# Kernel optimization log

Measured on AMD Instinct MI355X. Metric: run time of the kernel, lower is better.

The kernel has to match this reference:

```python
import jax, jax.numpy as jnp
import numpy as np
from jax import lax

B, NP = 4, 8192          # events, points per event (equal-sized batches)
RATIO, R, K = 0.25, 0.2, 64
MP = int(NP * RATIO)     # sampled centers per event
D_IN = 32
BIG = 1e10


def _fps_one(pos):
    # Farthest point sampling (deterministic start at index 0). pos: [NP,3] -> [MP] int32
    d = jnp.sum((pos - pos[0]) ** 2, axis=-1)
    sel = jnp.zeros((MP,), jnp.int32)

    def body(i, carry):
        sel, d = carry
        nxt = jnp.argmax(d).astype(jnp.int32)
        sel = sel.at[i].set(nxt)
        d = jnp.minimum(d, jnp.sum((pos - pos[nxt]) ** 2, axis=-1))
        return sel, d

    sel, _ = lax.fori_loop(1, MP, body, (sel, d))
    return sel


def _ball_query_one(centers, pos):
    # centers: [MP,3], pos: [NP,3] -> neighbor idx [MP,K] int32, validity mask [MP,K]
    d2 = jnp.sum((centers[:, None, :] - pos[None, :, :]) ** 2, axis=-1)  # [MP,NP]
    d2m = jnp.where(d2 <= R * R, d2, BIG)
    neg, idx = lax.top_k(-d2m, K)          # K nearest within radius (deterministic)
    mask = (-neg) <= R * R
    return idx.astype(jnp.int32), mask


def reference(x, pos, batch, W1, b1, W2, b2, W3, b3):
    xb = x.reshape(B, NP, D_IN)
    pb = pos.reshape(B, NP, 3)

    sel = jax.vmap(_fps_one)(pb)                                   # [B,MP]
    centers = jnp.take_along_axis(pb, sel[..., None], axis=1)      # [B,MP,3]
    idx, mask = jax.vmap(_ball_query_one)(centers, pb)             # [B,MP,K]

    gather = jax.vmap(lambda a, i: a[i])
    pos_j = gather(pb, idx)                                        # [B,MP,K,3]
    x_j = gather(xb, idx)                                          # [B,MP,K,D_IN]

    rel = pos_j - centers[:, :, None, :]
    h = jnp.concatenate([x_j, rel], axis=-1)                       # [B,MP,K,D_IN+3]
    h = jax.nn.relu(h @ W1 + b1)
    h = jax.nn.relu(h @ W2 + b2)
    h = jax.nn.relu(h @ W3 + b3)                                   # [B,MP,K,128]

    h = jnp.where(mask[..., None], h, -BIG)
    x_out = jnp.max(h, axis=2).reshape(B * MP, -1)                 # max aggregation
    pos_out = centers.reshape(B * MP, 3)
    batch_out = jnp.repeat(jnp.arange(B, dtype=jnp.int32), MP)
    return x_out, pos_out, batch_out


def setup_inputs() -> dict:
    key = jax.random.key(0)
    ks = jax.random.split(key, 8)
    x = jax.random.normal(ks[0], (B * NP, D_IN), jnp.float32)
    pos = jax.random.uniform(ks[1], (B * NP, 3), jnp.float32)
    batch = (jnp.arange(B * NP) // NP).astype(jnp.int64)
    W1 = jax.random.normal(ks[2], (D_IN + 3, 64), jnp.float32) * 0.05
    b1 = jnp.zeros((64,), jnp.float32)
    W2 = jax.random.normal(ks[3], (64, 64), jnp.float32) * 0.05
    b2 = jnp.zeros((64,), jnp.float32)
    W3 = jax.random.normal(ks[4], (64, 128), jnp.float32) * 0.05
    b3 = jnp.zeros((128,), jnp.float32)
    return {"x": x, "pos": pos, "batch": batch, "W1": W1, "b1": b1,
            "W2": W2, "b2": b2, "W3": W3, "b3": b3}
```

## Files before the change

### kernel.cpp

```cpp
#include <hip/hip_runtime.h>


#define BATCH 4
#define NP 8192
#define MP 2048
#define KNN 64
#define DIN 32
#define PPL 32

#define DPP_FMAX(v, ctrl)                                                     \
  {                                                                           \
    int _t = __builtin_amdgcn_update_dpp(__float_as_int(v),                   \
                                         __float_as_int(v), (ctrl), 0xF,      \
                                         0xF, false);                         \
    (v) = fmaxf((v), __int_as_float(_t));                                     \
  }

#define DPP_MINU(v, ctrl)                                                     \
  {                                                                           \
    unsigned _t = (unsigned)__builtin_amdgcn_update_dpp((int)(v), (int)(v),   \
                                                        (ctrl), 0xF, 0xF,    \
                                                        false);               \
    (v) = ((v) < _t) ? (v) : _t;                                              \
  }

typedef float v2f __attribute__((ext_vector_type(2)));

__global__ __launch_bounds__(256, 1) void fps_k(const float* __restrict__ pos,
                                                const float* __restrict__ x,
                                                const float* __restrict__ W1,
                                                const float* __restrict__ W2,
                                                const float* __restrict__ W3,
                                                float* __restrict__ pout,
                                                float* __restrict__ bout,
                                                float* __restrict__ P1,
                                                float* __restrict__ W2T,
                                                float* __restrict__ W3T)
{
  const int bid = blockIdx.x;
  const int tid = threadIdx.x;

  if (bid >= BATCH) {
    if (bid < BATCH + 8192) {
      const int j = (bid - BATCH) * 4 + (tid >> 6);
      const int c = tid & 63;
      const float* __restrict__ xr = x + (size_t)j * DIN;
      float acc = 0.f;
#pragma unroll
      for (int k = 0; k < DIN; k++) acc += xr[k] * W1[k * 64 + c];
      P1[(size_t)j * 64 + c] = acc;
    } else {
      const int e = (bid - (BATCH + 8192)) * 256 + tid;
      if (e < 64 * 64) {
        const int c = e >> 6, k = e & 63;
        W2T[e] = W2[k * 64 + c];
      } else {
        const int e2 = e - 64 * 64;
        const int c = e2 >> 6, k = e2 & 63;
        W3T[e2] = W3[k * 128 + c];
      }
    }
    return;
  }

  const int b = bid;
  const int lane = tid & 63, wid = tid >> 6;
  const float* __restrict__ pb = pos + (size_t)b * NP * 3;
  const int base = tid * PPL;

#pragma unroll
  for (int q = 0; q < 8; q++) bout[b * MP + q * 256 + tid] = (float)b;

  __shared__ __align__(16) float ptab[NP * 3];
  __shared__ unsigned long long slt[2][4];

  {
    float4* __restrict__ pt4 = (float4*)ptab;
    const float4* __restrict__ pv4 = (const float4*)pb;
#pragma unroll
    for (int q = 0; q < 24; q++) pt4[q * 256 + tid] = pv4[q * 256 + tid];
  }

  const float c0x = pb[0], c0y = pb[1], c0z = pb[2];
  if (tid == 0) {
    pout[(size_t)b * MP * 3 + 0] = c0x;
    pout[(size_t)b * MP * 3 + 1] = c0y;
    pout[(size_t)b * MP * 3 + 2] = c0z;
  }
  __syncthreads();

  v2f px[16], py[16], pz[16], d[16];
#pragma unroll
  for (int j = 0; j < 16; j++) {
    const float* __restrict__ pp = &ptab[tid * (PPL * 3) + j * 6];
    const v2f A = *(const v2f*)&pp[0];
    const v2f Bv = *(const v2f*)&pp[2];
    const v2f C = *(const v2f*)&pp[4];
    px[j].x = A.x;  px[j].y = Bv.y;
    py[j].x = A.y;  py[j].y = C.x;
    pz[j].x = Bv.x; pz[j].y = C.y;
  }

  float bv = -1.f;
  {
    const v2f cx = {c0x, c0x}, cy = {c0y, c0y}, cz = {c0z, c0z};
#pragma unroll
    for (int j = 0; j < 16; j++) {
      v2f dx = px[j] - cx, dy = py[j] - cy, dz = pz[j] - cz;
      v2f nd = dx * dx + dy * dy + dz * dz;
      d[j] = nd;
      bv = fmaxf(fmaxf(nd.x, nd.y), bv);
    }
  }

  for (int i = 1; i < MP; i++) {
    float v = bv;
    DPP_FMAX(v, 0x111);
    DPP_FMAX(v, 0x112);
    DPP_FMAX(v, 0x114);
    DPP_FMAX(v, 0x118);
    DPP_FMAX(v, 0x142);
    DPP_FMAX(v, 0x143);
    const float wmax =
        __int_as_float(__builtin_amdgcn_readlane(__float_as_int(v), 63));

    const unsigned long long m = __ballot(bv == wmax);
    const int src = (int)__builtin_ctzll(m);
    const int p = i & 1;
    if (lane == src) {
      int ks = PPL - 1;
#pragma unroll
      for (int k = PPL - 2; k >= 0; k--) {
        const float dv = (k & 1) ? d[k >> 1].y : d[k >> 1].x;
        if (dv == wmax) ks = k;
      }
      slt[p][wid] = ((unsigned long long)__float_as_uint(wmax) << 32)
                    | (unsigned)(base + ks);
    }
    __syncthreads();

    const unsigned long long kv = slt[p][lane & 3];
    const float v2 = __uint_as_float((unsigned)(kv >> 32));
    float v2r = v2;
    DPP_FMAX(v2r, 0x111);
    DPP_FMAX(v2r, 0x112);
    const float mv =
        __int_as_float(__builtin_amdgcn_readlane(__float_as_int(v2r), 3));
    const unsigned long long m2 = __ballot(v2 == mv);
    const int mw = (int)__builtin_ctzll(m2);
    const int js = __builtin_amdgcn_readlane((int)(unsigned)kv, mw);
    const float ncx = ptab[js * 3 + 0];
    const float ncy = ptab[js * 3 + 1];
    const float ncz = ptab[js * 3 + 2];

    if (tid == 0) {
      pout[((size_t)b * MP + i) * 3 + 0] = ncx;
      pout[((size_t)b * MP + i) * 3 + 1] = ncy;
      pout[((size_t)b * MP + i) * 3 + 2] = ncz;
    }

    const v2f cx = {ncx, ncx}, cy = {ncy, ncy}, cz = {ncz, ncz};
    bv = -1.f;
#pragma unroll
    for (int j = 0; j < 16; j++) {
      v2f dx = px[j] - cx, dy = py[j] - cy, dz = pz[j] - cz;
      v2f nd = dx * dx + dy * dy + dz * dz;
      v2f dn;
      dn.x = fminf(d[j].x, nd.x);
      dn.y = fminf(d[j].y, nd.y);
      d[j] = dn;
      bv = fmaxf(fmaxf(dn.x, dn.y), bv);
    }
  }
}

__global__ __launch_bounds__(64) void ballq_k(const float* __restrict__ pos,
                                              const float* __restrict__ pout,
                                              int* __restrict__ nbr)
{
  const int wg = blockIdx.x;
  const int lane = threadIdx.x;
  const int b = wg >> 11;
  const float* __restrict__ pb = pos + (size_t)b * NP * 3;
  const float cx = pout[(size_t)wg * 3 + 0];
  const float cy = pout[(size_t)wg * 3 + 1];
  const float cz = pout[(size_t)wg * 3 + 2];
  const float R2 = (float)(0.2 * 0.2);

  __shared__ unsigned long long cand[1024];
  int cnt = 0;
  for (int basej = 0; basej < NP; basej += 64) {
    const int j = basej + lane;
    float dx = pb[j * 3 + 0] - cx;
    float dy = pb[j * 3 + 1] - cy;
    float dz = pb[j * 3 + 2] - cz;
    float d2 = dx * dx + dy * dy + dz * dz;
    bool in = (d2 <= R2);
    unsigned long long mb = __ballot(in);
    int pre = (int)__popcll(mb & ((1ull << lane) - 1ull));
    int slot = cnt + pre;
    if (in && slot < 1024)
      cand[slot] = ((unsigned long long)__float_as_uint(d2) << 32) | (unsigned int)j;
    cnt += (int)__popcll(mb);
  }
  if (cnt > 1024) cnt = 1024;

  unsigned long long last = 0;
  int myout = -1;
  for (int r = 0; r < KNN; r++) {
    unsigned long long v = ~0ull;
    for (int s = lane; s < cnt; s += 64) {
      const unsigned long long c = cand[s];
      if (c >= last && c < v) v = c;
    }
    const unsigned hi = (unsigned)(v >> 32);
    unsigned h = hi;
    DPP_MINU(h, 0x111);
    DPP_MINU(h, 0x112);
    DPP_MINU(h, 0x114);
    DPP_MINU(h, 0x118);
    DPP_MINU(h, 0x142);
    DPP_MINU(h, 0x143);
    const unsigned mhi = (unsigned)__builtin_amdgcn_readlane((int)h, 63);
    const unsigned lo = (hi == mhi) ? (unsigned)v : 0xffffffffu;
    unsigned l2 = lo;
    DPP_MINU(l2, 0x111);
    DPP_MINU(l2, 0x112);
    DPP_MINU(l2, 0x114);
    DPP_MINU(l2, 0x118);
    DPP_MINU(l2, 0x142);
    DPP_MINU(l2, 0x143);
    const unsigned mlo = (unsigned)__builtin_amdgcn_readlane((int)l2, 63);

    if (lane == r) myout = (mhi == 0xffffffffu) ? -1 : (int)mlo;
    last = (mhi == 0xffffffffu)
               ? ~0ull
               : ((((unsigned long long)mhi << 32) | mlo) + 1ull);
  }
  nbr[(size_t)wg * KNN + lane] = myout;
}

__global__ __launch_bounds__(64) void mlp_k(const float* __restrict__ pos,
    const float* __restrict__ P1, const float* __restrict__ W1,
    const float* __restrict__ b1, const float* __restrict__ W2T,
    const float* __restrict__ b2, const float* __restrict__ W3T,
    const float* __restrict__ b3, const int* __restrict__ nbr,
    const float* __restrict__ pout, float* __restrict__ xout)
{
  __shared__ __align__(16) float h2s[64 * 68];
  const int wg = blockIdx.x;
  const int lane = threadIdx.x;
  const int b = wg >> 11;
  const int idx = nbr[(size_t)wg * KNN + lane];
  const bool valid = idx >= 0;
  const int j = valid ? idx : 0;
  const float cx = pout[(size_t)wg * 3 + 0];
  const float cy = pout[(size_t)wg * 3 + 1];
  const float cz = pout[(size_t)wg * 3 + 2];
  const float* __restrict__ pj = pos + ((size_t)b * NP + j) * 3;
  const float rx = pj[0] - cx, ry = pj[1] - cy, rz = pj[2] - cz;
  const float* __restrict__ p1r =
      (const float*)__builtin_assume_aligned(P1 + ((size_t)b * NP + j) * 64, 16);

  float h1[64];
#pragma unroll
  for (int k = 0; k < 64; k++) {
    float v = p1r[k] + rx * W1[32 * 64 + k] + ry * W1[33 * 64 + k]
                     + rz * W1[34 * 64 + k] + b1[k];
    h1[k] = fmaxf(v, 0.f);
  }

  for (int c4 = 0; c4 < 16; c4++) {
    float a0 = b2[c4 * 4 + 0], a1 = b2[c4 * 4 + 1];
    float a2 = b2[c4 * 4 + 2], a3 = b2[c4 * 4 + 3];
    const float* __restrict__ w0 = W2T + (c4 * 4 + 0) * 64;
    const float* __restrict__ w1 = W2T + (c4 * 4 + 1) * 64;
    const float* __restrict__ w2 = W2T + (c4 * 4 + 2) * 64;
    const float* __restrict__ w3 = W2T + (c4 * 4 + 3) * 64;
#pragma unroll
    for (int k = 0; k < 64; k++) {
      a0 += h1[k] * w0[k]; a1 += h1[k] * w1[k];
      a2 += h1[k] * w2[k]; a3 += h1[k] * w3[k];
    }
    float4 q;
    q.x = fmaxf(a0, 0.f); q.y = fmaxf(a1, 0.f);
    q.z = fmaxf(a2, 0.f); q.w = fmaxf(a3, 0.f);
    *(float4*)&h2s[lane * 68 + c4 * 4] = q;
  }

  float4 keep = make_float4(0.f, 0.f, 0.f, 0.f);
  const float* __restrict__ h2p = &h2s[lane * 68];
  for (int c4 = 0; c4 < 32; c4++) {
    float a0 = b3[c4 * 4 + 0], a1 = b3[c4 * 4 + 1];
    float a2 = b3[c4 * 4 + 2], a3 = b3[c4 * 4 + 3];
    const float* __restrict__ w0 = W3T + (c4 * 4 + 0) * 64;
    const float* __restrict__ w1 = W3T + (c4 * 4 + 1) * 64;
    const float* __restrict__ w2 = W3T + (c4 * 4 + 2) * 64;
    const float* __restrict__ w3 = W3T + (c4 * 4 + 3) * 64;
#pragma unroll
    for (int k4 = 0; k4 < 16; k4++) {
      float4 h = *(const float4*)&h2p[k4 * 4];
      a0 += h.x * w0[k4 * 4 + 0]; a0 += h.y * w0[k4 * 4 + 1];
      a0 += h.z * w0[k4 * 4 + 2]; a0 += h.w * w0[k4 * 4 + 3];
      a1 += h.x * w1[k4 * 4 + 0]; a1 += h.y * w1[k4 * 4 + 1];
      a1 += h.z * w1[k4 * 4 + 2]; a1 += h.w * w1[k4 * 4 + 3];
      a2 += h.x * w2[k4 * 4 + 0]; a2 += h.y * w2[k4 * 4 + 1];
      a2 += h.z * w2[k4 * 4 + 2]; a2 += h.w * w2[k4 * 4 + 3];
      a3 += h.x * w3[k4 * 4 + 0]; a3 += h.y * w3[k4 * 4 + 1];
      a3 += h.z * w3[k4 * 4 + 2]; a3 += h.w * w3[k4 * 4 + 3];
    }
    a0 = valid ? fmaxf(a0, 0.f) : 0.f;
    a1 = valid ? fmaxf(a1, 0.f) : 0.f;
    a2 = valid ? fmaxf(a2, 0.f) : 0.f;
    a3 = valid ? fmaxf(a3, 0.f) : 0.f;
#pragma unroll
    for (int off = 1; off < 64; off <<= 1) {
      a0 = fmaxf(a0, __shfl_xor(a0, off));
      a1 = fmaxf(a1, __shfl_xor(a1, off));
      a2 = fmaxf(a2, __shfl_xor(a2, off));
      a3 = fmaxf(a3, __shfl_xor(a3, off));
    }
    if (lane == c4) { keep.x = a0; keep.y = a1; keep.z = a2; keep.w = a3; }
  }
  if (lane < 32)
    *(float4*)&xout[(size_t)wg * 128 + lane * 4] = keep;
}

extern "C" void kernel_launch(void* const* d_in, const int* in_sizes, int n_in,
                              void* d_out, int out_size, void* d_ws, size_t ws_size,
                              hipStream_t stream)
{
  const float* x   = (const float*)d_in[0];
  const float* pos = (const float*)d_in[1];
  const float* W1 = (const float*)d_in[3];
  const float* b1 = (const float*)d_in[4];
  const float* W2 = (const float*)d_in[5];
  const float* b2 = (const float*)d_in[6];
  const float* W3 = (const float*)d_in[7];
  const float* b3 = (const float*)d_in[8];

  float* out  = (float*)d_out;
  float* xout = out;
  float* pout = out + 8192 * 128;
  float* bout = out + 8192 * 128 + 8192 * 3;

  char* ws = (char*)d_ws;
  float* P1  = (float*)ws;
  float* W2T = (float*)(ws + 8388608);
  float* W3T = (float*)(ws + 8404992);
  int*   nbr = (int*)(ws + 8437760);

  fps_k<<<dim3(BATCH + 8192 + 48), dim3(256), 0, stream>>>(
      pos, x, W1, W2, W3, pout, bout, P1, W2T, W3T);
  ballq_k<<<dim3(BATCH * MP), dim3(64), 0, stream>>>(pos, pout, nbr);
  mlp_k<<<dim3(BATCH * MP), dim3(64), 0, stream>>>(pos, P1, W1, b1, W2T, b2,
                                                   W3T, b3, nbr, pout, xout);
}
```

Before: 2.693 ms.

## Widen FPS to 1024 threads per event and fuse ball query with MLP

Farthest point sampling now uses 1024 threads per event, 8 points each, instead of 256 threads with 32 points each. This cuts the per-iteration serial distance update and argmax scan, at the cost of a wider 16-wave cross-wave reduction. The ball-query and MLP kernels are merged into one, with shared memory reused between them, so the neighbor index buffer round trip and one launch go away. The P1 precompute and weight-transpose blocks are regridded to match the 1024-thread block size.

```diff
diff --git a/kernel.cpp b/kernel.cpp
--- a/kernel.cpp
+++ b/kernel.cpp
@@ -6,7 +6,6 @@
 #define MP 2048
 #define KNN 64
 #define DIN 32
-#define PPL 32
 
 #define DPP_FMAX(v, ctrl)                                                     \
   {                                                                           \
@@ -26,23 +25,23 @@
 
 typedef float v2f __attribute__((ext_vector_type(2)));
 
-__global__ __launch_bounds__(256, 1) void fps_k(const float* __restrict__ pos,
-                                                const float* __restrict__ x,
-                                                const float* __restrict__ W1,
-                                                const float* __restrict__ W2,
-                                                const float* __restrict__ W3,
-                                                float* __restrict__ pout,
-                                                float* __restrict__ bout,
-                                                float* __restrict__ P1,
-                                                float* __restrict__ W2T,
-                                                float* __restrict__ W3T)
+__global__ __launch_bounds__(1024) void fps_k(const float* __restrict__ pos,
+                                              const float* __restrict__ x,
+                                              const float* __restrict__ W1,
+                                              const float* __restrict__ W2,
+                                              const float* __restrict__ W3,
+                                              float* __restrict__ pout,
+                                              float* __restrict__ bout,
+                                              float* __restrict__ P1,
+                                              float* __restrict__ W2T,
+                                              float* __restrict__ W3T)
 {
   const int bid = blockIdx.x;
   const int tid = threadIdx.x;
 
   if (bid >= BATCH) {
-    if (bid < BATCH + 8192) {
-      const int j = (bid - BATCH) * 4 + (tid >> 6);
+    if (bid < BATCH + 2048) {
+      const int j = (bid - BATCH) * 16 + (tid >> 6);
       const int c = tid & 63;
       const float* __restrict__ xr = x + (size_t)j * DIN;
       float acc = 0.f;
@@ -50,14 +49,17 @@
       for (int k = 0; k < DIN; k++) acc += xr[k] * W1[k * 64 + c];
       P1[(size_t)j * 64 + c] = acc;
     } else {
-      const int e = (bid - (BATCH + 8192)) * 256 + tid;
-      if (e < 64 * 64) {
-        const int c = e >> 6, k = e & 63;
-        W2T[e] = W2[k * 64 + c];
-      } else {
-        const int e2 = e - 64 * 64;
-        const int c = e2 >> 6, k = e2 & 63;
-        W3T[e2] = W3[k * 128 + c];
+#pragma unroll
+      for (int it = 0; it < 12; it++) {
+        const int e = it * 1024 + tid;
+        if (e < 64 * 64) {
+          const int c = e >> 6, k = e & 63;
+          W2T[e] = W2[k * 64 + c];
+        } else {
+          const int e2 = e - 64 * 64;
+          const int c = e2 >> 6, k = e2 & 63;
+          W3T[e2] = W3[k * 128 + c];
+        }
       }
     }
     return;
@@ -66,19 +68,26 @@
   const int b = bid;
   const int lane = tid & 63, wid = tid >> 6;
   const float* __restrict__ pb = pos + (size_t)b * NP * 3;
-  const int base = tid * PPL;
-
-#pragma unroll
-  for (int q = 0; q < 8; q++) bout[b * MP + q * 256 + tid] = (float)b;
+  const int base = tid * 8;
+
+  bout[b * MP + tid] = (float)b;
+  bout[b * MP + 1024 + tid] = (float)b;
 
   __shared__ __align__(16) float ptab[NP * 3];
-  __shared__ unsigned long long slt[2][4];
-
-  {
-    float4* __restrict__ pt4 = (float4*)ptab;
-    const float4* __restrict__ pv4 = (const float4*)pb;
-#pragma unroll
-    for (int q = 0; q < 24; q++) pt4[q * 256 + tid] = pv4[q * 256 + tid];
+  __shared__ unsigned long long slt[2][16];
+
+  float t[24];
+  const float4* __restrict__ pv = (const float4*)(pb + (size_t)tid * 24);
+#pragma unroll
+  for (int q = 0; q < 6; q++) *(float4*)&t[q * 4] = pv[q];
+#pragma unroll
+  for (int q = 0; q < 6; q++) *(float4*)&ptab[tid * 24 + q * 4] = *(float4*)&t[q * 4];
+
+  v2f px[4], py[4], pz[4], d[4];
+#pragma unroll
+  for (int j = 0; j < 4; j++) {
+    px[j].x = t[6 * j + 0]; py[j].x = t[6 * j + 1]; pz[j].x = t[6 * j + 2];
+    px[j].y = t[6 * j + 3]; py[j].y = t[6 * j + 4]; pz[j].y = t[6 * j + 5];
   }
 
   const float c0x = pb[0], c0y = pb[1], c0z = pb[2];
@@ -87,29 +96,16 @@
     pout[(size_t)b * MP * 3 + 1] = c0y;
     pout[(size_t)b * MP * 3 + 2] = c0z;
   }
-  __syncthreads();
-
-  v2f px[16], py[16], pz[16], d[16];
-#pragma unroll
-  for (int j = 0; j < 16; j++) {
-    const float* __restrict__ pp = &ptab[tid * (PPL * 3) + j * 6];
-    const v2f A = *(const v2f*)&pp[0];
-    const v2f Bv = *(const v2f*)&pp[2];
-    const v2f C = *(const v2f*)&pp[4];
-    px[j].x = A.x;  px[j].y = Bv.y;
-    py[j].x = A.y;  py[j].y = C.x;
-    pz[j].x = Bv.x; pz[j].y = C.y;
-  }
 
   float bv = -1.f;
   {
-    const v2f cx = {c0x, c0x}, cy = {c0y, c0y}, cz = {c0z, c0z};
-#pragma unroll
-    for (int j = 0; j < 16; j++) {
+    v2f cx = {c0x, c0x}, cy = {c0y, c0y}, cz = {c0z, c0z};
+#pragma unroll
+    for (int j = 0; j < 4; j++) {
       v2f dx = px[j] - cx, dy = py[j] - cy, dz = pz[j] - cz;
       v2f nd = dx * dx + dy * dy + dz * dz;
       d[j] = nd;
-      bv = fmaxf(fmaxf(nd.x, nd.y), bv);
+      bv = fmaxf(bv, fmaxf(nd.x, nd.y));
     }
   }
 
@@ -128,10 +124,10 @@
     const int src = (int)__builtin_ctzll(m);
     const int p = i & 1;
     if (lane == src) {
-      int ks = PPL - 1;
-#pragma unroll
-      for (int k = PPL - 2; k >= 0; k--) {
-        const float dv = (k & 1) ? d[k >> 1].y : d[k >> 1].x;
+      int ks = 7;
+#pragma unroll
+      for (int k = 6; k >= 0; k--) {
+        float dv = (k & 1) ? d[k >> 1].y : d[k >> 1].x;
         if (dv == wmax) ks = k;
       }
       slt[p][wid] = ((unsigned long long)__float_as_uint(wmax) << 32)
@@ -139,13 +135,15 @@
     }
     __syncthreads();
 
-    const unsigned long long kv = slt[p][lane & 3];
+    const unsigned long long kv = slt[p][lane & 15];
     const float v2 = __uint_as_float((unsigned)(kv >> 32));
     float v2r = v2;
     DPP_FMAX(v2r, 0x111);
     DPP_FMAX(v2r, 0x112);
+    DPP_FMAX(v2r, 0x114);
+    DPP_FMAX(v2r, 0x118);
     const float mv =
-        __int_as_float(__builtin_amdgcn_readlane(__float_as_int(v2r), 3));
+        __int_as_float(__builtin_amdgcn_readlane(__float_as_int(v2r), 15));
     const unsigned long long m2 = __ballot(v2 == mv);
     const int mw = (int)__builtin_ctzll(m2);
     const int js = __builtin_amdgcn_readlane((int)(unsigned)kv, mw);
@@ -162,22 +160,28 @@
     const v2f cx = {ncx, ncx}, cy = {ncy, ncy}, cz = {ncz, ncz};
     bv = -1.f;
 #pragma unroll
-    for (int j = 0; j < 16; j++) {
+    for (int j = 0; j < 4; j++) {
       v2f dx = px[j] - cx, dy = py[j] - cy, dz = pz[j] - cz;
       v2f nd = dx * dx + dy * dy + dz * dz;
       v2f dn;
       dn.x = fminf(d[j].x, nd.x);
       dn.y = fminf(d[j].y, nd.y);
       d[j] = dn;
-      bv = fmaxf(fmaxf(dn.x, dn.y), bv);
+      bv = fmaxf(bv, fmaxf(dn.x, dn.y));
     }
   }
 }
 
-__global__ __launch_bounds__(64) void ballq_k(const float* __restrict__ pos,
-                                              const float* __restrict__ pout,
-                                              int* __restrict__ nbr)
+__global__ __launch_bounds__(64) void bqmlp_k(const float* __restrict__ pos,
+    const float* __restrict__ P1, const float* __restrict__ W1,
+    const float* __restrict__ b1, const float* __restrict__ W2T,
+    const float* __restrict__ b2, const float* __restrict__ W3T,
+    const float* __restrict__ b3, const float* __restrict__ pout,
+    float* __restrict__ xout)
 {
+  __shared__ __align__(16) float smem[64 * 68];
+  unsigned long long* __restrict__ cand = (unsigned long long*)smem;
+
   const int wg = blockIdx.x;
   const int lane = threadIdx.x;
   const int b = wg >> 11;
@@ -187,7 +191,6 @@
   const float cz = pout[(size_t)wg * 3 + 2];
   const float R2 = (float)(0.2 * 0.2);
 
-  __shared__ unsigned long long cand[1024];
   int cnt = 0;
   for (int basej = 0; basej < NP; basej += 64) {
     const int j = basej + lane;
@@ -237,26 +240,12 @@
                ? ~0ull
                : ((((unsigned long long)mhi << 32) | mlo) + 1ull);
   }
-  nbr[(size_t)wg * KNN + lane] = myout;
-}
-
-__global__ __launch_bounds__(64) void mlp_k(const float* __restrict__ pos,
-    const float* __restrict__ P1, const float* __restrict__ W1,
-    const float* __restrict__ b1, const float* __restrict__ W2T,
-    const float* __restrict__ b2, const float* __restrict__ W3T,
-    const float* __restrict__ b3, const int* __restrict__ nbr,
-    const float* __restrict__ pout, float* __restrict__ xout)
-{
-  __shared__ __align__(16) float h2s[64 * 68];
-  const int wg = blockIdx.x;
-  const int lane = threadIdx.x;
-  const int b = wg >> 11;
-  const int idx = nbr[(size_t)wg * KNN + lane];
+
+  __syncthreads();
+
+  const int idx = myout;
   const bool valid = idx >= 0;
   const int j = valid ? idx : 0;
-  const float cx = pout[(size_t)wg * 3 + 0];
-  const float cy = pout[(size_t)wg * 3 + 1];
-  const float cz = pout[(size_t)wg * 3 + 2];
   const float* __restrict__ pj = pos + ((size_t)b * NP + j) * 3;
   const float rx = pj[0] - cx, ry = pj[1] - cy, rz = pj[2] - cz;
   const float* __restrict__ p1r =
@@ -285,11 +274,11 @@
     float4 q;
     q.x = fmaxf(a0, 0.f); q.y = fmaxf(a1, 0.f);
     q.z = fmaxf(a2, 0.f); q.w = fmaxf(a3, 0.f);
-    *(float4*)&h2s[lane * 68 + c4 * 4] = q;
+    *(float4*)&smem[lane * 68 + c4 * 4] = q;
   }
 
   float4 keep = make_float4(0.f, 0.f, 0.f, 0.f);
-  const float* __restrict__ h2p = &h2s[lane * 68];
+  const float* __restrict__ h2p = &smem[lane * 68];
   for (int c4 = 0; c4 < 32; c4++) {
     float a0 = b3[c4 * 4 + 0], a1 = b3[c4 * 4 + 1];
     float a2 = b3[c4 * 4 + 2], a3 = b3[c4 * 4 + 3];
@@ -348,11 +337,9 @@
   float* P1  = (float*)ws;
   float* W2T = (float*)(ws + 8388608);
   float* W3T = (float*)(ws + 8404992);
-  int*   nbr = (int*)(ws + 8437760);
-
-  fps_k<<<dim3(BATCH + 8192 + 48), dim3(256), 0, stream>>>(
+
+  fps_k<<<dim3(BATCH + 2048 + 1), dim3(1024), 0, stream>>>(
       pos, x, W1, W2, W3, pout, bout, P1, W2T, W3T);
-  ballq_k<<<dim3(BATCH * MP), dim3(64), 0, stream>>>(pos, pout, nbr);
-  mlp_k<<<dim3(BATCH * MP), dim3(64), 0, stream>>>(pos, P1, W1, b1, W2T, b2,
-                                                   W3T, b3, nbr, pout, xout);
+  bqmlp_k<<<dim3(BATCH * MP), dim3(64), 0, stream>>>(pos, P1, W1, b1, W2T, b2,
+                                                     W3T, b3, pout, xout);
 }
```

Result: faster. 2.625 ms (-2.5%).
